# Optimization experiments

Measured on AMD Instinct MI355X. Metric: run time of the kernel, lower is better.

Reference implementation:

```python
import jax, jax.numpy as jnp
import numpy as np

NUM_CLASSES = 90
ALPHA = 0.5
GAMMA = 2.0
EPS = 1e-4


def _calc_iou(a, b):
    # a: [A,4] anchors in (y1,x1,y2,x2); b: [M,4] gt boxes in (x1,y1,x2,y2)
    area = (b[:, 2] - b[:, 0]) * (b[:, 3] - b[:, 1])  # [M]
    iw = jnp.minimum(a[:, 3, None], b[None, :, 2]) - jnp.maximum(a[:, 1, None], b[None, :, 0])
    ih = jnp.minimum(a[:, 2, None], b[None, :, 3]) - jnp.maximum(a[:, 0, None], b[None, :, 1])
    iw = jnp.clip(iw, 0.0)
    ih = jnp.clip(ih, 0.0)
    ua = ((a[:, 2] - a[:, 0]) * (a[:, 3] - a[:, 1]))[:, None] + area[None, :] - iw * ih
    ua = jnp.clip(ua, 1e-8)
    return (iw * ih) / ua  # [A,M]


def _per_image_loss(cls, reg, ann, anchor, anchor_w, anchor_h, anchor_cx, anchor_cy):
    # cls: [A,C]; reg: [A,4]; ann: [M,5]
    valid = ann[:, 4] != -1.0  # [M]
    p = jnp.clip(cls, EPS, 1.0 - EPS)
    iou = _calc_iou(anchor, ann[:, :4])
    iou = jnp.where(valid[None, :], iou, -1.0)
    iou_max = jnp.max(iou, axis=1)              # [A]
    iou_argmax = jnp.argmax(iou, axis=1)        # [A]

    pos = iou_max >= 0.5                         # [A]
    num_pos = jnp.sum(pos)
    base = jnp.where((iou_max < 0.4) | pos, 0.0, -1.0)[:, None]  # [A,1]
    assigned = ann[iou_argmax]                   # [A,5]
    lbl = assigned[:, 4].astype(jnp.int32)
    onehot = (jnp.arange(NUM_CLASSES)[None, :] == lbl[:, None]) & pos[:, None]
    targets = jnp.where(onehot, 1.0, base)       # [A,C] in {-1,0,1}

    # focal BCE
    is_one = targets == 1.0
    alpha_factor = jnp.where(is_one, ALPHA, 1.0 - ALPHA)
    focal_w = alpha_factor * jnp.where(is_one, 1.0 - p, p) ** GAMMA
    bce = -(targets * jnp.log(p) + (1.0 - targets) * jnp.log(1.0 - p))
    cls_loss = jnp.where(targets != -1.0, focal_w * bce, 0.0)
    npos_f = num_pos.astype(p.dtype)
    cls_l = jnp.sum(cls_loss) / jnp.maximum(npos_f, 1.0)

    gt_w = assigned[:, 2] - assigned[:, 0]
    gt_h = assigned[:, 3] - assigned[:, 1]
    gt_cx = assigned[:, 0] + 0.5 * gt_w
    gt_cy = assigned[:, 1] + 0.5 * gt_h
    gt_w = jnp.clip(gt_w, 1.0)
    gt_h = jnp.clip(gt_h, 1.0)
    t_dx = (gt_cx - anchor_cx) / anchor_w
    t_dy = (gt_cy - anchor_cy) / anchor_h
    t_dw = jnp.log(gt_w / anchor_w)
    t_dh = jnp.log(gt_h / anchor_h)
    t = jnp.stack((t_dy, t_dx, t_dh, t_dw), axis=1)  # [A,4]
    diff = jnp.abs(t - reg)
    rl = jnp.where(diff <= 1.0 / 9.0, 0.5 * 9.0 * diff * diff, diff - 0.5 / 9.0)
    rl = jnp.where(pos[:, None], rl, 0.0)
    reg_l = jnp.where(num_pos > 0,
                      jnp.sum(rl) / jnp.maximum(npos_f * 4.0, 1.0),
                      jnp.zeros((), p.dtype))
    return cls_l, reg_l


def reference(classifications, regressions, anchors, annotations):
    anchor = anchors[0]  # [A,4] (y1,x1,y2,x2)
    aw = anchor[:, 3] - anchor[:, 1]
    ah = anchor[:, 2] - anchor[:, 0]
    acx = anchor[:, 1] + 0.5 * aw
    acy = anchor[:, 0] + 0.5 * ah
    cls_l, reg_l = jax.vmap(
        lambda c, r, a: _per_image_loss(c, r, a, anchor, aw, ah, acx, acy)
    )(classifications, regressions, annotations)
    # mode='mean'
    return (jnp.mean(cls_l, keepdims=True), jnp.mean(reg_l, keepdims=True))


def setup_inputs() -> dict:
    key = jax.random.key(0)
    k1, k2, k3, k4, k5, k6, k7 = jax.random.split(key, 7)
    B, A, C, M = 8, 49104, 90, 32
    classifications = jax.random.uniform(k1, (B, A, C), jnp.float32, 0.001, 0.999)
    regressions = jax.random.normal(k2, (B, A, 4), jnp.float32)
    # anchors in (y1,x1,y2,x2)
    ctr = jax.random.uniform(k3, (A, 2), jnp.float32, 16.0, 496.0)  # (cy,cx)
    wh = jax.random.uniform(k4, (A, 2), jnp.float32, 16.0, 128.0)   # (h,w)
    anchor = jnp.concatenate([ctr - 0.5 * wh, ctr + 0.5 * wh], axis=1)  # y1,x1,y2,x2
    anchors = anchor[None]  # [1,A,4]
    # annotations in (x1,y1,x2,y2,label), all valid
    gctr = jax.random.uniform(k5, (B, M, 2), jnp.float32, 64.0, 448.0)  # (cx,cy)
    gwh = jax.random.uniform(k6, (B, M, 2), jnp.float32, 32.0, 160.0)   # (w,h)
    boxes = jnp.concatenate([gctr - 0.5 * gwh, gctr + 0.5 * gwh], axis=2)
    labels = jax.random.randint(k7, (B, M, 1), 0, C).astype(jnp.float32)
    annotations = jnp.concatenate([boxes, labels], axis=2)
    return {"classifications": classifications, "regressions": regressions,
            "anchors": anchors, "annotations": annotations}
```

## Files before the change

kernel.cpp:

```cpp
#include <hip/hip_runtime.h>
#include <stdint.h>

#define NB 8
#define NA 49104
#define NC 90
#define NM 32
#define APB 256
#define GX ((NA + APB - 1) / APB)
#define CPB (APB * NC / 4)
#define CHUNKS_IMG (NA * NC / 4)
#define LN2_HALF 0.34657359027997264

typedef float f32x4 __attribute__((ext_vector_type(4)));


template<int N>
__device__ inline void load_group(const f32x4* __restrict__ ci, int gbase,
                                  int cstart, int t,
                                  f32x4* v, float* wm, int* cl)
{
    #pragma unroll
    for (int u = 0; u < N; ++u) {
        const int c = cstart + u * 256 + t;
        const bool ok = c < CPB;
        wm[u] = ok ? 1.0f : 0.0f;
        cl[u] = ok ? c : 0;
        v[u] = ci[gbase + cl[u]];
    }
}

template<int N>
__device__ inline float compute_group(const f32x4* v, const float* wm,
                                      const int* cl,
                                      const float* s_w, const int* s_t)
{
    float acc = 0.0f;
    #pragma unroll
    for (int u = 0; u < N; ++u) {
        const int e0   = cl[u] * 4;
        const int aidl = (e0 * 46604) >> 22;
        const int c0   = e0 - aidl * 90;
        const float w0 = s_w[aidl]     * wm[u];
        const float w1 = s_w[aidl + 1] * wm[u];
        const int   t0 = s_t[aidl];
        const int   t1 = s_t[aidl + 1] + 90;
        const float pv[4] = {v[u].x, v[u].y, v[u].z, v[u].w};
        #pragma unroll
        for (int j = 0; j < 4; ++j) {
            const int cc   = c0 + j;
            const bool inA = cc < 90;
            const float w  = inA ? w0 : w1;
            const int  tgt = inA ? t0 : t1;
            const float p  = pv[j];
            const float q  = 1.0f - p;
            const bool hit = (cc == tgt);
            const float a  = hit ? q : p;
            const float bb = hit ? p : q;
            acc = fmaf(a * a * __log2f(bb), w, acc);
        }
    }
    return acc;
}

__global__ __launch_bounds__(256, 4) void fl_fused(
    const float* __restrict__ anchors,
    const f32x4* __restrict__ cls,
    const float* __restrict__ regressions,
    const float* __restrict__ annotations,
    float* __restrict__ cls_p,
    float* __restrict__ reg_p,
    int* __restrict__ np_p)
{
    const int bx = blockIdx.x;
    const int b  = blockIdx.y;
    const int t  = threadIdx.x;

    __shared__ float s_ann[NM * 5];
    __shared__ float s_w[APB + 1];
    __shared__ int   s_t[APB + 1];

    if (t < NM * 5)
        s_ann[t] = annotations[b * NM * 5 + t];
    __syncthreads();

    const int a = bx * APB + t;
    float rsum = 0.0f;
    int   pcnt = 0;
    float wv = 0.0f;
    int   tv = 0x7fff;

    if (a < NA) {
        const f32x4 av = ((const f32x4*)anchors)[a];
        const float ay1 = av.x, ax1 = av.y, ay2 = av.z, ax2 = av.w;
        const float aw = ax2 - ax1, ah = ay2 - ay1;
        const float aarea = aw * ah;

        float best = -2.0f;
        int bm = 0;
        #pragma unroll 4
        for (int m = 0; m < NM; ++m) {
            const float bx1 = s_ann[m * 5 + 0];
            const float by1 = s_ann[m * 5 + 1];
            const float bx2 = s_ann[m * 5 + 2];
            const float by2 = s_ann[m * 5 + 3];
            const float lab = s_ann[m * 5 + 4];
            const float area = (bx2 - bx1) * (by2 - by1);
            float iw = fminf(ax2, bx2) - fmaxf(ax1, bx1);
            float ih = fminf(ay2, by2) - fmaxf(ay1, by1);
            iw = fmaxf(iw, 0.0f);
            ih = fmaxf(ih, 0.0f);
            const float inter = iw * ih;
            const float ua = fmaxf(aarea + area - inter, 1e-8f);
            float iou = inter / ua;
            if (lab == -1.0f) iou = -1.0f;
            if (iou > best) { best = iou; bm = m; }
        }

        const bool pos = best >= 0.5f;
        const bool bz  = (best < 0.4f) || pos;
        wv = bz ? 1.0f : 0.0f;
        tv = pos ? (((int)s_ann[bm * 5 + 4]) & 0x7f) : 0x7fff;

        if (pos) {
            pcnt = 1;
            const float bx1 = s_ann[bm * 5 + 0];
            const float by1 = s_ann[bm * 5 + 1];
            const float bx2 = s_ann[bm * 5 + 2];
            const float by2 = s_ann[bm * 5 + 3];
            float gw = bx2 - bx1, gh = by2 - by1;
            const float gcx = bx1 + 0.5f * gw;
            const float gcy = by1 + 0.5f * gh;
            gw = fmaxf(gw, 1.0f);
            gh = fmaxf(gh, 1.0f);
            const float acx = ax1 + 0.5f * aw;
            const float acy = ay1 + 0.5f * ah;

            const f32x4 rv = ((const f32x4*)regressions)[(size_t)b * NA + a];
            const float t0 = (gcy - acy) / ah;
            const float t1 = (gcx - acx) / aw;
            const float t2 = logf(gh / ah);
            const float t3 = logf(gw / aw);

            float d;
            d = fabsf(t0 - rv.x); rsum += (d <= 1.0f/9.0f) ? 4.5f*d*d : d - 1.0f/18.0f;
            d = fabsf(t1 - rv.y); rsum += (d <= 1.0f/9.0f) ? 4.5f*d*d : d - 1.0f/18.0f;
            d = fabsf(t2 - rv.z); rsum += (d <= 1.0f/9.0f) ? 4.5f*d*d : d - 1.0f/18.0f;
            d = fabsf(t3 - rv.w); rsum += (d <= 1.0f/9.0f) ? 4.5f*d*d : d - 1.0f/18.0f;
        }
    }

    s_w[t] = wv;
    s_t[t] = tv;
    if (t == 0) { s_w[APB] = 0.0f; s_t[APB] = 0x7fff; }
    __syncthreads();

    const f32x4* ci = cls + (size_t)b * CHUNKS_IMG;
    const int gbase = bx * CPB;

    f32x4 vA[8], vB[8];
    float wmA[8], wmB[8];
    int   clA[8], clB[8];

    load_group<8>(ci, gbase, 0,    t, vA, wmA, clA);
    load_group<8>(ci, gbase, 2048, t, vB, wmB, clB);
    float acc = compute_group<8>(vA, wmA, clA, s_w, s_t);
    load_group<7>(ci, gbase, 4096, t, vA, wmA, clA);
    acc += compute_group<8>(vB, wmB, clB, s_w, s_t);
    acc += compute_group<7>(vA, wmA, clA, s_w, s_t);

    #pragma unroll
    for (int off = 32; off; off >>= 1) {
        acc  += __shfl_down(acc, off);
        rsum += __shfl_down(rsum, off);
        pcnt += __shfl_down(pcnt, off);
    }
    __shared__ float sa[4], sr[4];
    __shared__ int   sp[4];
    const int wid = t >> 6;
    if ((t & 63) == 0) { sa[wid] = acc; sr[wid] = rsum; sp[wid] = pcnt; }
    __syncthreads();
    if (t == 0) {
        const int slot = b * GX + bx;
        cls_p[slot] = sa[0] + sa[1] + sa[2] + sa[3];
        reg_p[slot] = sr[0] + sr[1] + sr[2] + sr[3];
        np_p[slot]  = sp[0] + sp[1] + sp[2] + sp[3];
    }
}

__global__ __launch_bounds__(256) void fl_final(
    const float* __restrict__ cls_p,
    const float* __restrict__ reg_p,
    const int* __restrict__ np_p,
    float* __restrict__ out)
{
    const int t = threadIdx.x;
    const int img = t >> 5, lane = t & 31;

    float cs = 0.0f, rs = 0.0f;
    int ns = 0;
    #pragma unroll
    for (int k = 0; k < GX / 32; ++k) {
        const int s = img * GX + k * 32 + lane;
        cs += cls_p[s];
        rs += reg_p[s];
        ns += np_p[s];
    }
    #pragma unroll
    for (int off = 16; off; off >>= 1) {
        cs += __shfl_down(cs, off);
        rs += __shfl_down(rs, off);
        ns += __shfl_down(ns, off);
    }
    __shared__ double s_c[8], s_r[8];
    __shared__ int    s_n[8];
    if (lane == 0) { s_c[img] = (double)cs; s_r[img] = (double)rs; s_n[img] = ns; }
    __syncthreads();
    if (t == 0) {
        double cl = 0.0, rl = 0.0;
        for (int b = 0; b < NB; ++b) {
            const int np = s_n[b];
            cl += s_c[b] * (-LN2_HALF) / (double)(np > 1 ? np : 1);
            if (np > 0) rl += s_r[b] / (4.0 * (double)np);
        }
        out[0] = (float)(cl / (double)NB);
        out[1] = (float)(rl / (double)NB);
    }
}

extern "C" void kernel_launch(void* const* d_in, const int* in_sizes, int n_in,
                              void* d_out, int out_size, void* d_ws, size_t ws_size,
                              hipStream_t stream) {
    const float* cls = (const float*)d_in[0];
    const float* reg = (const float*)d_in[1];
    const float* anc = (const float*)d_in[2];
    const float* ann = (const float*)d_in[3];
    float* out = (float*)d_out;

    char* ws = (char*)d_ws;
    float* cls_p = (float*)(ws + 0);
    float* reg_p = (float*)(ws + 8192);
    int*   np_p  = (int*)(ws + 16384);

    dim3 g(GX, NB);
    fl_fused<<<g, 256, 0, stream>>>(anc, (const f32x4*)cls, reg, ann,
                                    cls_p, reg_p, np_p);
    fl_final<<<1, 256, 0, stream>>>(cls_p, reg_p, np_p, out);
}
```

Before: 214.4 us.

## Compute focal loss as all-negative sum plus per-positive correction term

The dense class loop now treats every class as a negative target, dropping the per-element target comparison and select logic and the s_t shared array. Each positive anchor adds a correction term that replaces its negative contribution with the positive one for its labelled class, loading one extra scalar probability. The correction is reduced into a new workspace slot and combined in the final kernel. The load/compute software pipelining across groups is also folded into one function per group, so overlap of loads with compute is left to the compiler.

```diff
diff --git a/kernel.cpp b/kernel.cpp
--- a/kernel.cpp
+++ b/kernel.cpp
@@ -15,10 +15,12 @@
 
 
 template<int N>
-__device__ inline void load_group(const f32x4* __restrict__ ci, int gbase,
-                                  int cstart, int t,
-                                  f32x4* v, float* wm, int* cl)
+__device__ inline float focal_group(const f32x4* __restrict__ ci, int gbase,
+                                    int cstart, int t, const float* s_w)
 {
+    f32x4 v[N];
+    int   cl[N];
+    float wm[N];
     #pragma unroll
     for (int u = 0; u < N; ++u) {
         const int c = cstart + u * 256 + t;
@@ -27,13 +29,6 @@
         cl[u] = ok ? c : 0;
         v[u] = ci[gbase + cl[u]];
     }
-}
-
-template<int N>
-__device__ inline float compute_group(const f32x4* v, const float* wm,
-                                      const int* cl,
-                                      const float* s_w, const int* s_t)
-{
     float acc = 0.0f;
     #pragma unroll
     for (int u = 0; u < N; ++u) {
@@ -42,21 +37,12 @@
         const int c0   = e0 - aidl * 90;
         const float w0 = s_w[aidl]     * wm[u];
         const float w1 = s_w[aidl + 1] * wm[u];
-        const int   t0 = s_t[aidl];
-        const int   t1 = s_t[aidl + 1] + 90;
         const float pv[4] = {v[u].x, v[u].y, v[u].z, v[u].w};
         #pragma unroll
         for (int j = 0; j < 4; ++j) {
-            const int cc   = c0 + j;
-            const bool inA = cc < 90;
-            const float w  = inA ? w0 : w1;
-            const int  tgt = inA ? t0 : t1;
-            const float p  = pv[j];
-            const float q  = 1.0f - p;
-            const bool hit = (cc == tgt);
-            const float a  = hit ? q : p;
-            const float bb = hit ? p : q;
-            acc = fmaf(a * a * __log2f(bb), w, acc);
+            const float w = (c0 + j < 90) ? w0 : w1;
+            const float p = pv[j];
+            acc = fmaf(p * p * __log2f(1.0f - p), w, acc);
         }
     }
     return acc;
@@ -69,7 +55,8 @@
     const float* __restrict__ annotations,
     float* __restrict__ cls_p,
     float* __restrict__ reg_p,
-    int* __restrict__ np_p)
+    int* __restrict__ np_p,
+    float* __restrict__ cor_p)
 {
     const int bx = blockIdx.x;
     const int b  = blockIdx.y;
@@ -77,7 +64,6 @@
 
     __shared__ float s_ann[NM * 5];
     __shared__ float s_w[APB + 1];
-    __shared__ int   s_t[APB + 1];
 
     if (t < NM * 5)
         s_ann[t] = annotations[b * NM * 5 + t];
@@ -85,9 +71,9 @@
 
     const int a = bx * APB + t;
     float rsum = 0.0f;
+    float csum = 0.0f;
     int   pcnt = 0;
     float wv = 0.0f;
-    int   tv = 0x7fff;
 
     if (a < NA) {
         const f32x4 av = ((const f32x4*)anchors)[a];
@@ -119,7 +105,6 @@
         const bool pos = best >= 0.5f;
         const bool bz  = (best < 0.4f) || pos;
         wv = bz ? 1.0f : 0.0f;
-        tv = pos ? (((int)s_ann[bm * 5 + 4]) & 0x7f) : 0x7fff;
 
         if (pos) {
             pcnt = 1;
@@ -146,43 +131,43 @@
             d = fabsf(t1 - rv.y); rsum += (d <= 1.0f/9.0f) ? 4.5f*d*d : d - 1.0f/18.0f;
             d = fabsf(t2 - rv.z); rsum += (d <= 1.0f/9.0f) ? 4.5f*d*d : d - 1.0f/18.0f;
             d = fabsf(t3 - rv.w); rsum += (d <= 1.0f/9.0f) ? 4.5f*d*d : d - 1.0f/18.0f;
+
+            const int L = ((int)s_ann[bm * 5 + 4]) & 0x7f;
+            const float pL = ((const float*)cls)[((size_t)b * NA + a) * NC + L];
+            const float qL = 1.0f - pL;
+            csum = 0.5f * (pL * pL * __logf(qL) - qL * qL * __logf(pL));
         }
     }
 
     s_w[t] = wv;
-    s_t[t] = tv;
-    if (t == 0) { s_w[APB] = 0.0f; s_t[APB] = 0x7fff; }
+    if (t == 0) s_w[APB] = 0.0f;
     __syncthreads();
 
     const f32x4* ci = cls + (size_t)b * CHUNKS_IMG;
     const int gbase = bx * CPB;
 
-    f32x4 vA[8], vB[8];
-    float wmA[8], wmB[8];
-    int   clA[8], clB[8];
-
-    load_group<8>(ci, gbase, 0,    t, vA, wmA, clA);
-    load_group<8>(ci, gbase, 2048, t, vB, wmB, clB);
-    float acc = compute_group<8>(vA, wmA, clA, s_w, s_t);
-    load_group<7>(ci, gbase, 4096, t, vA, wmA, clA);
-    acc += compute_group<8>(vB, wmB, clB, s_w, s_t);
-    acc += compute_group<7>(vA, wmA, clA, s_w, s_t);
+    float acc;
+    acc  = focal_group<8>(ci, gbase, 0,    t, s_w);
+    acc += focal_group<8>(ci, gbase, 2048, t, s_w);
+    acc += focal_group<7>(ci, gbase, 4096, t, s_w);
 
     #pragma unroll
     for (int off = 32; off; off >>= 1) {
         acc  += __shfl_down(acc, off);
         rsum += __shfl_down(rsum, off);
+        csum += __shfl_down(csum, off);
         pcnt += __shfl_down(pcnt, off);
     }
-    __shared__ float sa[4], sr[4];
+    __shared__ float sa[4], sr[4], sc[4];
     __shared__ int   sp[4];
     const int wid = t >> 6;
-    if ((t & 63) == 0) { sa[wid] = acc; sr[wid] = rsum; sp[wid] = pcnt; }
+    if ((t & 63) == 0) { sa[wid] = acc; sr[wid] = rsum; sc[wid] = csum; sp[wid] = pcnt; }
     __syncthreads();
     if (t == 0) {
         const int slot = b * GX + bx;
         cls_p[slot] = sa[0] + sa[1] + sa[2] + sa[3];
         reg_p[slot] = sr[0] + sr[1] + sr[2] + sr[3];
+        cor_p[slot] = sc[0] + sc[1] + sc[2] + sc[3];
         np_p[slot]  = sp[0] + sp[1] + sp[2] + sp[3];
     }
 }
@@ -191,35 +176,41 @@
     const float* __restrict__ cls_p,
     const float* __restrict__ reg_p,
     const int* __restrict__ np_p,
+    const float* __restrict__ cor_p,
     float* __restrict__ out)
 {
     const int t = threadIdx.x;
     const int img = t >> 5, lane = t & 31;
 
-    float cs = 0.0f, rs = 0.0f;
+    float cs = 0.0f, rs = 0.0f, cr = 0.0f;
     int ns = 0;
     #pragma unroll
     for (int k = 0; k < GX / 32; ++k) {
         const int s = img * GX + k * 32 + lane;
         cs += cls_p[s];
         rs += reg_p[s];
+        cr += cor_p[s];
         ns += np_p[s];
     }
     #pragma unroll
     for (int off = 16; off; off >>= 1) {
         cs += __shfl_down(cs, off);
         rs += __shfl_down(rs, off);
+        cr += __shfl_down(cr, off);
         ns += __shfl_down(ns, off);
     }
-    __shared__ double s_c[8], s_r[8];
+    __shared__ double s_c[8], s_r[8], s_x[8];
     __shared__ int    s_n[8];
-    if (lane == 0) { s_c[img] = (double)cs; s_r[img] = (double)rs; s_n[img] = ns; }
+    if (lane == 0) {
+        s_c[img] = (double)cs; s_r[img] = (double)rs;
+        s_x[img] = (double)cr; s_n[img] = ns;
+    }
     __syncthreads();
     if (t == 0) {
         double cl = 0.0, rl = 0.0;
         for (int b = 0; b < NB; ++b) {
             const int np = s_n[b];
-            cl += s_c[b] * (-LN2_HALF) / (double)(np > 1 ? np : 1);
+            cl += (s_c[b] * (-LN2_HALF) + s_x[b]) / (double)(np > 1 ? np : 1);
             if (np > 0) rl += s_r[b] / (4.0 * (double)np);
         }
         out[0] = (float)(cl / (double)NB);
@@ -240,9 +231,10 @@
     float* cls_p = (float*)(ws + 0);
     float* reg_p = (float*)(ws + 8192);
     int*   np_p  = (int*)(ws + 16384);
+    float* cor_p = (float*)(ws + 24576);
 
     dim3 g(GX, NB);
     fl_fused<<<g, 256, 0, stream>>>(anc, (const f32x4*)cls, reg, ann,
-                                    cls_p, reg_p, np_p);
-    fl_final<<<1, 256, 0, stream>>>(cls_p, reg_p, np_p, out);
-}
+                                    cls_p, reg_p, np_p, cor_p);
+    fl_final<<<1, 256, 0, stream>>>(cls_p, reg_p, np_p, cor_p, out);
+}
```

Result: no change. 214.3 us (-0.1%).
